# Kernel optimization log

Measured on AMD Instinct MI355X. Metric: run time of the kernel, lower is better.

## Reference

```python
import jax, jax.numpy as jnp
import numpy as np

N, D, B, C, T, TOD = 8192, 32, 2, 8, 12, 288
PARAM_SCALE = 0.3  # keep relu+softmax logits well-conditioned (original uses plain randn init)


def setup_inputs() -> dict:
    key = jax.random.key(0)
    k0, k1, k2, k3, k4 = jax.random.split(key, 5)
    return {
        "x": jax.random.normal(k0, (B, C, N, T), dtype=jnp.float32),
        "nodevec1": PARAM_SCALE * jax.random.normal(k1, (N, D), dtype=jnp.float32),
        "nodevec2": PARAM_SCALE * jax.random.normal(k2, (N, D), dtype=jnp.float32),
        "timevec": PARAM_SCALE * jax.random.normal(k3, (TOD, D), dtype=jnp.float32),
        "k": PARAM_SCALE * jax.random.normal(k4, (D, D, D), dtype=jnp.float32),
        "time_ind": 100,
    }


def reference(x, nodevec1, nodevec2, timevec, k, time_ind):
    # Dynamic Tucker-decomposition adjacency (SpatialGraphConv.forward, eval mode -> dropout is identity)
    tv = timevec[time_ind]                             # [D]   time_vec
    core = jnp.einsum('d,def->ef', tv, k)              # [D,D] adp1 (squeezed)
    # adp2/adp3 chain: (nodevec1 @ core) @ nodevec2.T  -> [N,N]
    adp = jnp.einsum('ne,ef->nf', nodevec1, core)      # [N,D]
    adp = jnp.einsum('nf,mf->nm', adp, nodevec2)       # [N,N]
    adp = jax.nn.softmax(jax.nn.relu(adp), axis=-1)    # row-softmax over neighbors
    # NConv: neighbor aggregation  'bcnt,nm->bcmt'
    return jnp.einsum('bcnt,nm->bcmt', x, adp)
```

## Files before the change

### kernel.cpp

```cpp
#include <hip/hip_runtime.h>
#include <hip/hip_bf16.h>


#define NN 8192
#define DD 32
#define TT 12
#define NSPLIT 8
#define CHUNK 1024

typedef __attribute__((ext_vector_type(8))) short bf16x8;
typedef __attribute__((ext_vector_type(4))) short bf16x4;
typedef __attribute__((ext_vector_type(4))) float f32x4;
typedef __attribute__((ext_vector_type(16))) float f32x16;

static __device__ __forceinline__ unsigned short f2bf(float f) {
  unsigned int u = __float_as_uint(f);
  u = (u + 0x7FFFu + ((u >> 16) & 1u)) >> 16;
  return (unsigned short)u;
}

static __device__ __forceinline__ unsigned int pk2(float lo, float hi) {
  return (unsigned int)f2bf(lo) | ((unsigned int)f2bf(hi) << 16);
}

static __device__ __forceinline__ float fexp2(float x) {
#if __has_builtin(__builtin_amdgcn_exp2f)
  return __builtin_amdgcn_exp2f(x);
#else
  return __builtin_exp2f(x);
#endif
}

__global__ __launch_bounds__(256) void k_prep(const float* __restrict__ nv1,
                                              const float* __restrict__ nv2,
                                              const float* __restrict__ timevec,
                                              const float* __restrict__ kk,
                                              const int* __restrict__ tind,
                                              unsigned short* __restrict__ t1b,
                                              unsigned short* __restrict__ nv2b,
                                              float* __restrict__ sums) {
  __shared__ float cs[1024];
  const int tid = threadIdx.x;
  if (tid < 128) sums[blockIdx.x * 128 + tid] = 0.f;
  const float* tv = timevec + (size_t)tind[0] * DD;
  for (int idx = tid; idx < 1024; idx += 256) {
    float acc = 0.f;
#pragma unroll
    for (int d = 0; d < DD; ++d) acc += tv[d] * kk[d * 1024 + idx];
    cs[idx] = acc;
  }
  __syncthreads();
  const int nbase = blockIdx.x * 128;
  const int f = tid & 31, sub = tid >> 5;
#pragma unroll 4
  for (int it = 0; it < 16; ++it) {
    const int n = nbase + it * 8 + sub;
    const float* nr = nv1 + (size_t)n * DD;
    float acc = 0.f;
#pragma unroll
    for (int e = 0; e < DD; ++e) acc += nr[e] * cs[e * DD + f];
    t1b[(size_t)n * DD + f] = f2bf(acc * 1.4426950408889634f);
  }
#pragma unroll 4
  for (int it = 0; it < 16; ++it) {
    const int idx = nbase * DD + it * 256 + tid;
    nv2b[idx] = f2bf(nv2[idx]);
  }
}

__global__ __launch_bounds__(256) void k_stats(const unsigned short* __restrict__ t1b,
                                               const unsigned short* __restrict__ nv2b,
                                               float* __restrict__ sums) {
  const int tid = threadIdx.x;
  const int w = tid >> 6, lane = tid & 63, q = lane >> 4, i16 = lane & 15;
  const int nbase = blockIdx.x * 64 + w * 16;
  bf16x8 a = *(const bf16x8*)(t1b + (size_t)(nbase + i16) * DD + q * 8);
  const f32x4 z4 = {0.f, 0.f, 0.f, 0.f};
  float s[4] = {0.f, 0.f, 0.f, 0.f};
  const int m0 = blockIdx.y * 1024;
  for (int mt = m0; mt < m0 + 1024; mt += 64) {
#pragma unroll
    for (int u = 0; u < 4; ++u) {
      bf16x8 b = *(const bf16x8*)(nv2b + (size_t)(mt + u * 16 + i16) * DD + q * 8);
      f32x4 d = __builtin_amdgcn_mfma_f32_16x16x32_bf16(a, b, z4, 0, 0, 0);
#pragma unroll
      for (int r = 0; r < 4; ++r) s[r] += fexp2(fmaxf(d[r], 0.f));
    }
  }
#pragma unroll
  for (int r = 0; r < 4; ++r)
    for (int off = 1; off < 16; off <<= 1) s[r] += __shfl_xor(s[r], off, 64);
  if (i16 == 0) {
#pragma unroll
    for (int r = 0; r < 4; ++r) atomicAdd(&sums[nbase + q * 4 + r], s[r]);
  }
}

__global__ __launch_bounds__(256) void k_y(const float* __restrict__ x,
                                           const float* __restrict__ sums,
                                           unsigned short* __restrict__ yT) {
  __shared__ float xs[3072];
  const int tid = threadIdx.x;
  const int n0 = blockIdx.x * 256;
  const int bc = blockIdx.y;
  const float* xp = x + (size_t)bc * NN * TT + (size_t)n0 * TT;
#pragma unroll
  for (int j = 0; j < 12; ++j) xs[j * 256 + tid] = xp[j * 256 + tid];
  __syncthreads();
  const float rinv = 1.0f / sums[n0 + tid];
#pragma unroll
  for (int t = 0; t < 12; ++t)
    yT[(size_t)(bc * TT + t) * NN + n0 + tid] = f2bf(xs[tid * 12 + t] * rinv);
}

__global__ __launch_bounds__(256, 2) void k_mega(const unsigned short* __restrict__ t1b,
                                                 const unsigned short* __restrict__ nv2b,
                                                 const unsigned short* __restrict__ yT,
                                                 float* __restrict__ part) {
  const int tid = threadIdx.x;
  const int w = tid >> 6, lane = tid & 63;
  const int h = lane >> 5, m31 = lane & 31;
  const int mw = blockIdx.x * 128 + w * 32;
  const int nt0 = blockIdx.y * CHUNK;

  bf16x8 bn0 = *(const bf16x8*)(nv2b + (size_t)(mw + m31) * DD + h * 8);
  bf16x8 bn1 = *(const bf16x8*)(nv2b + (size_t)(mw + m31) * DD + 16 + h * 8);

  f32x16 acc[6];
#pragma unroll
  for (int c = 0; c < 6; ++c)
#pragma unroll
    for (int r = 0; r < 16; ++r) acc[c][r] = 0.f;
  f32x16 z16;
#pragma unroll
  for (int r = 0; r < 16; ++r) z16[r] = 0.f;

  bf16x8 ta0 = *(const bf16x8*)(t1b + (size_t)(nt0 + m31) * DD + h * 8);
  bf16x8 ta1 = *(const bf16x8*)(t1b + (size_t)(nt0 + m31) * DD + 16 + h * 8);

  for (int nt = nt0; nt < nt0 + CHUNK; nt += 32) {
    bf16x8 yf[6][2];
#pragma unroll
    for (int c = 0; c < 6; ++c) {
      const unsigned short* yp = yT + (size_t)(c * 32 + m31) * NN + nt + h * 8;
      yf[c][0] = *(const bf16x8*)(yp);
      yf[c][1] = *(const bf16x8*)(yp + 16);
    }

    f32x16 d = __builtin_amdgcn_mfma_f32_32x32x16_bf16(ta1, bn1, z16, 0, 0, 0);
    d = __builtin_amdgcn_mfma_f32_32x32x16_bf16(ta0, bn0, d, 0, 0, 0);

    if (nt + 32 < nt0 + CHUNK) {
      ta0 = *(const bf16x8*)(t1b + (size_t)(nt + 32 + m31) * DD + h * 8);
      ta1 = *(const bf16x8*)(t1b + (size_t)(nt + 32 + m31) * DD + 16 + h * 8);
    }

    float e[16];
#pragma unroll
    for (int r = 0; r < 16; ++r) e[r] = fexp2(fmaxf(d[r], 0.f));

    unsigned int frag[2][4];
#pragma unroll
    for (int kh = 0; kh < 2; ++kh) {
#pragma unroll
      for (int b = 0; b < 4; b += 2) {
        unsigned int P0 = pk2(e[8 * kh + b], e[8 * kh + b + 1]);
        unsigned int P1 = pk2(e[8 * kh + 4 + b], e[8 * kh + 5 + b]);
        unsigned int S0 = __shfl_xor(P0, 32, 64);
        unsigned int S1 = __shfl_xor(P1, 32, 64);
        frag[kh][b >> 1] = h ? S1 : P0;
        frag[kh][2 + (b >> 1)] = h ? P1 : S0;
      }
    }
    bf16x8 ef0, ef1;
    __builtin_memcpy(&ef0, &frag[0][0], 16);
    __builtin_memcpy(&ef1, &frag[1][0], 16);

#pragma unroll
    for (int c = 0; c < 6; ++c) {
      acc[c] = __builtin_amdgcn_mfma_f32_32x32x16_bf16(yf[c][0], ef0, acc[c], 0, 0, 0);
      acc[c] = __builtin_amdgcn_mfma_f32_32x32x16_bf16(yf[c][1], ef1, acc[c], 0, 0, 0);
    }
  }

  float* pp = part + (size_t)blockIdx.y * 192 * NN;
#pragma unroll
  for (int c = 0; c < 6; ++c)
#pragma unroll
    for (int r = 0; r < 16; ++r) {
      const int col = c * 32 + (r & 3) + 8 * (r >> 2) + 4 * h;
      pp[(size_t)col * NN + mw + m31] = acc[c][r];
    }
}

__global__ __launch_bounds__(256) void k_reduce(const float* __restrict__ part,
                                                float* __restrict__ out) {
  __shared__ float os[3072];
  const int tid = threadIdx.x;
  const int m0 = blockIdx.x * 256;
  const int bc = blockIdx.y;
#pragma unroll
  for (int t = 0; t < 12; ++t) {
    const int col = bc * TT + t;
    float s = 0.f;
#pragma unroll
    for (int nc = 0; nc < NSPLIT; ++nc)
      s += part[((size_t)nc * 192 + col) * NN + m0 + tid];
    os[tid * 12 + t] = s;
  }
  __syncthreads();
  float* op = out + (size_t)bc * NN * TT + (size_t)m0 * TT;
#pragma unroll
  for (int j = 0; j < 12; ++j) op[j * 256 + tid] = os[j * 256 + tid];
}

extern "C" void kernel_launch(void* const* d_in, const int* in_sizes, int n_in,
                              void* d_out, int out_size, void* d_ws, size_t ws_size,
                              hipStream_t stream) {
  const float* x = (const float*)d_in[0];
  const float* nv1 = (const float*)d_in[1];
  const float* nv2 = (const float*)d_in[2];
  const float* tv = (const float*)d_in[3];
  const float* kk = (const float*)d_in[4];
  const int* tind = (const int*)d_in[5];
  float* out = (float*)d_out;

  char* ws = (char*)d_ws;
  unsigned short* t1b  = (unsigned short*)(ws);
  unsigned short* nv2b = (unsigned short*)(ws + 524288);
  float* sums          = (float*)(ws + 1048576);
  unsigned short* yT   = (unsigned short*)(ws + 1081344);
  float* part          = (float*)(ws + 4227072);

  k_prep<<<64, 256, 0, stream>>>(nv1, nv2, tv, kk, tind, t1b, nv2b, sums);
  k_stats<<<dim3(128, 8), 256, 0, stream>>>(t1b, nv2b, sums);
  k_y<<<dim3(32, 16), 256, 0, stream>>>(x, sums, yT);
  k_mega<<<dim3(64, NSPLIT), 256, 0, stream>>>(t1b, nv2b, yT, part);
  k_reduce<<<dim3(32, 16), 256, 0, stream>>>(part, out);
}
```

Measured before the change: 213.8 us.

## Split mega kernel into producer and consumer warps sharing exp tiles via LDS ring

The fused attention-style kernel now uses 512 threads: four producer waves compute the relu/exp2 score tiles with MFMA and write bf16 results into a 3-slot swizzled LDS ring buffer. Four consumer waves load y fragments and run the aggregation MFMAs on those tiles, with spin-wait flags in LDS for handshaking. This is meant to overlap the transcendental and packing work with the matrix accumulation, and to drop the cross-lane shuffle repacking. In exchange it adds spin-wait synchronisation, LDS traffic and a different occupancy profile.

```diff
diff --git a/kernel.cpp b/kernel.cpp
--- a/kernel.cpp
+++ b/kernel.cpp
@@ -7,6 +7,7 @@
 #define TT 12
 #define NSPLIT 8
 #define CHUNK 1024
+#define RSLOT 3
 
 typedef __attribute__((ext_vector_type(8))) short bf16x8;
 typedef __attribute__((ext_vector_type(4))) short bf16x4;
@@ -17,10 +18,6 @@
   unsigned int u = __float_as_uint(f);
   u = (u + 0x7FFFu + ((u >> 16) & 1u)) >> 16;
   return (unsigned short)u;
-}
-
-static __device__ __forceinline__ unsigned int pk2(float lo, float hi) {
-  return (unsigned int)f2bf(lo) | ((unsigned int)f2bf(hi) << 16);
 }
 
 static __device__ __forceinline__ float fexp2(float x) {
@@ -113,84 +110,113 @@
     yT[(size_t)(bc * TT + t) * NN + n0 + tid] = f2bf(xs[tid * 12 + t] * rinv);
 }
 
-__global__ __launch_bounds__(256, 2) void k_mega(const unsigned short* __restrict__ t1b,
-                                                 const unsigned short* __restrict__ nv2b,
-                                                 const unsigned short* __restrict__ yT,
-                                                 float* __restrict__ part) {
+__global__ __launch_bounds__(512) void k_mega(const unsigned short* __restrict__ t1b,
+                                              const unsigned short* __restrict__ nv2b,
+                                              const unsigned short* __restrict__ yT,
+                                              float* __restrict__ part) {
+  __shared__ unsigned short Et[RSLOT][128][64];
+  __shared__ int flg[2 * RSLOT];
   const int tid = threadIdx.x;
   const int w = tid >> 6, lane = tid & 63;
-  const int h = lane >> 5, m31 = lane & 31;
-  const int mw = blockIdx.x * 128 + w * 32;
+  const int h = lane >> 5, l31 = lane & 31;
+  const int mb = blockIdx.x * 128;
   const int nt0 = blockIdx.y * CHUNK;
-
-  bf16x8 bn0 = *(const bf16x8*)(nv2b + (size_t)(mw + m31) * DD + h * 8);
-  bf16x8 bn1 = *(const bf16x8*)(nv2b + (size_t)(mw + m31) * DD + 16 + h * 8);
-
-  f32x16 acc[6];
-#pragma unroll
-  for (int c = 0; c < 6; ++c)
-#pragma unroll
-    for (int r = 0; r < 16; ++r) acc[c][r] = 0.f;
-  f32x16 z16;
-#pragma unroll
-  for (int r = 0; r < 16; ++r) z16[r] = 0.f;
-
-  bf16x8 ta0 = *(const bf16x8*)(t1b + (size_t)(nt0 + m31) * DD + h * 8);
-  bf16x8 ta1 = *(const bf16x8*)(t1b + (size_t)(nt0 + m31) * DD + 16 + h * 8);
-
-  for (int nt = nt0; nt < nt0 + CHUNK; nt += 32) {
-    bf16x8 yf[6][2];
-#pragma unroll
-    for (int c = 0; c < 6; ++c) {
-      const unsigned short* yp = yT + (size_t)(c * 32 + m31) * NN + nt + h * 8;
-      yf[c][0] = *(const bf16x8*)(yp);
-      yf[c][1] = *(const bf16x8*)(yp + 16);
-    }
-
-    f32x16 d = __builtin_amdgcn_mfma_f32_32x32x16_bf16(ta1, bn1, z16, 0, 0, 0);
-    d = __builtin_amdgcn_mfma_f32_32x32x16_bf16(ta0, bn0, d, 0, 0, 0);
-
-    if (nt + 32 < nt0 + CHUNK) {
-      ta0 = *(const bf16x8*)(t1b + (size_t)(nt + 32 + m31) * DD + h * 8);
-      ta1 = *(const bf16x8*)(t1b + (size_t)(nt + 32 + m31) * DD + 16 + h * 8);
-    }
-
-    float e[16];
-#pragma unroll
-    for (int r = 0; r < 16; ++r) e[r] = fexp2(fmaxf(d[r], 0.f));
-
-    unsigned int frag[2][4];
-#pragma unroll
-    for (int kh = 0; kh < 2; ++kh) {
-#pragma unroll
-      for (int b = 0; b < 4; b += 2) {
-        unsigned int P0 = pk2(e[8 * kh + b], e[8 * kh + b + 1]);
-        unsigned int P1 = pk2(e[8 * kh + 4 + b], e[8 * kh + 5 + b]);
-        unsigned int S0 = __shfl_xor(P0, 32, 64);
-        unsigned int S1 = __shfl_xor(P1, 32, 64);
-        frag[kh][b >> 1] = h ? S1 : P0;
-        frag[kh][2 + (b >> 1)] = h ? P1 : S0;
-      }
-    }
-    bf16x8 ef0, ef1;
-    __builtin_memcpy(&ef0, &frag[0][0], 16);
-    __builtin_memcpy(&ef1, &frag[1][0], 16);
-
-#pragma unroll
-    for (int c = 0; c < 6; ++c) {
-      acc[c] = __builtin_amdgcn_mfma_f32_32x32x16_bf16(yf[c][0], ef0, acc[c], 0, 0, 0);
-      acc[c] = __builtin_amdgcn_mfma_f32_32x32x16_bf16(yf[c][1], ef1, acc[c], 0, 0, 0);
-    }
-  }
-
-  float* pp = part + (size_t)blockIdx.y * 192 * NN;
-#pragma unroll
-  for (int c = 0; c < 6; ++c)
-#pragma unroll
-    for (int r = 0; r < 16; ++r) {
-      const int col = c * 32 + (r & 3) + 8 * (r >> 2) + 4 * h;
-      pp[(size_t)col * NN + mw + m31] = acc[c][r];
-    }
+  const int swz = (l31 & 7) << 3;
+  if (tid < 2 * RSLOT) flg[tid] = 0;
+  __syncthreads();
+  volatile int* vflg = flg;
+
+  if (w < 4) {
+    const int p = w;
+    bf16x8 bn0 = *(const bf16x8*)(nv2b + (size_t)(mb + p * 32 + l31) * DD + h * 8);
+    bf16x8 bn1 = *(const bf16x8*)(nv2b + (size_t)(mb + p * 32 + l31) * DD + 16 + h * 8);
+    f32x16 z16;
+#pragma unroll
+    for (int r = 0; r < 16; ++r) z16[r] = 0.f;
+
+    bf16x8 at[4], nx[4];
+#pragma unroll
+    for (int ns = 0; ns < 2; ++ns) {
+      const size_t rowb = (size_t)(nt0 + ns * 32 + l31) * DD;
+      at[ns * 2 + 0] = *(const bf16x8*)(t1b + rowb + h * 8);
+      at[ns * 2 + 1] = *(const bf16x8*)(t1b + rowb + 16 + h * 8);
+    }
+    for (int st = 0; st < 16; ++st) {
+      const int s = st % RSLOT;
+      const int occ = st / RSLOT;
+      if (st < 15) {
+#pragma unroll
+        for (int ns = 0; ns < 2; ++ns) {
+          const size_t rowb = (size_t)(nt0 + (st + 1) * 64 + ns * 32 + l31) * DD;
+          nx[ns * 2 + 0] = *(const bf16x8*)(t1b + rowb + h * 8);
+          nx[ns * 2 + 1] = *(const bf16x8*)(t1b + rowb + 16 + h * 8);
+        }
+      }
+      if (occ > 0) {
+        const int tgt = 4 * occ;
+        while (vflg[RSLOT + s] < tgt) __builtin_amdgcn_s_sleep(1);
+      }
+      __threadfence_block();
+#pragma unroll
+      for (int ns = 0; ns < 2; ++ns) {
+        f32x16 d = __builtin_amdgcn_mfma_f32_32x32x16_bf16(at[ns * 2 + 1], bn1, z16, 0, 0, 0);
+        d = __builtin_amdgcn_mfma_f32_32x32x16_bf16(at[ns * 2 + 0], bn0, d, 0, 0, 0);
+#pragma unroll
+        for (int g = 0; g < 4; ++g) {
+          bf16x4 ev;
+#pragma unroll
+          for (int b = 0; b < 4; ++b)
+            ev[b] = (short)f2bf(fexp2(fmaxf(d[4 * g + b], 0.f)));
+          *(bf16x4*)&Et[s][p * 32 + l31][(ns * 32 + 8 * g + 4 * h) ^ swz] = ev;
+        }
+      }
+      __threadfence_block();
+      if (lane == 0) atomicAdd(&flg[s], 1);
+#pragma unroll
+      for (int r = 0; r < 4; ++r) at[r] = nx[r];
+    }
+  } else {
+    const int c = w - 4;
+    f32x16 acc[6];
+#pragma unroll
+    for (int ct = 0; ct < 6; ++ct)
+#pragma unroll
+      for (int r = 0; r < 16; ++r) acc[ct][r] = 0.f;
+
+    for (int st = 0; st < 16; ++st) {
+      const int s = st % RSLOT;
+      const int tgt = 4 * (st / RSLOT + 1);
+      const int nb = nt0 + st * 64;
+      bf16x8 yf[6][4];
+#pragma unroll
+      for (int ct = 0; ct < 6; ++ct) {
+        const unsigned short* yp = yT + (size_t)(ct * 32 + l31) * NN + nb + h * 8;
+#pragma unroll
+        for (int ks = 0; ks < 4; ++ks) yf[ct][ks] = *(const bf16x8*)(yp + ks * 16);
+      }
+      while (vflg[s] < tgt) __builtin_amdgcn_s_sleep(1);
+      __threadfence_block();
+      bf16x8 bf[4];
+#pragma unroll
+      for (int ks = 0; ks < 4; ++ks)
+        bf[ks] = *(const bf16x8*)&Et[s][c * 32 + l31][(ks * 16 + h * 8) ^ swz];
+#pragma unroll
+      for (int ct = 0; ct < 6; ++ct)
+#pragma unroll
+        for (int ks = 0; ks < 4; ++ks)
+          acc[ct] = __builtin_amdgcn_mfma_f32_32x32x16_bf16(yf[ct][ks], bf[ks], acc[ct], 0, 0, 0);
+      __threadfence_block();
+      if (lane == 0) atomicAdd(&flg[RSLOT + s], 1);
+    }
+    float* pp = part + (size_t)blockIdx.y * 192 * NN;
+#pragma unroll
+    for (int ct = 0; ct < 6; ++ct)
+#pragma unroll
+      for (int r = 0; r < 16; ++r) {
+        const int col = ct * 32 + (r & 3) + 8 * (r >> 2) + 4 * h;
+        pp[(size_t)col * NN + mb + c * 32 + l31] = acc[ct][r];
+      }
+  }
 }
 
 __global__ __launch_bounds__(256) void k_reduce(const float* __restrict__ part,
@@ -235,6 +261,6 @@
   k_prep<<<64, 256, 0, stream>>>(nv1, nv2, tv, kk, tind, t1b, nv2b, sums);
   k_stats<<<dim3(128, 8), 256, 0, stream>>>(t1b, nv2b, sums);
   k_y<<<dim3(32, 16), 256, 0, stream>>>(x, sums, yT);
-  k_mega<<<dim3(64, NSPLIT), 256, 0, stream>>>(t1b, nv2b, yT, part);
+  k_mega<<<dim3(64, NSPLIT), 512, 0, stream>>>(t1b, nv2b, yT, part);
   k_reduce<<<dim3(32, 16), 256, 0, stream>>>(part, out);
 }
```

After: 218.6 us. 1.02x slower.
